# Kernel tuning notes

Measured on AMD Instinct MI355X. Metric: run time of the kernel, lower is better.

The kernel has to match this reference:

```python
import jax, jax.numpy as jnp
import numpy as np

H = 1024   # hidden_size (BERT-large)
B = 16     # bsz
L = 4      # num_label
S = 512    # seq len per (doc, option) pair
NEG = -1e30


def setup_inputs() -> dict:
    key = jax.random.key(0)
    ks = jax.random.split(key, 16)
    last_layer = jax.random.normal(ks[0], (B * L, S, H), dtype=jnp.float32)
    attention_mask = jnp.ones((B * L, S), dtype=jnp.int32)
    all_doc_final_pos = (300 + jax.random.randint(ks[1], (B * L,), 0, 150)).astype(jnp.int64)

    def w(k, shape, std=0.02):
        return jax.random.normal(k, shape, dtype=jnp.float32) * std

    return {
        "last_layer": last_layer,
        "attention_mask": attention_mask,
        "all_doc_final_pos": all_doc_final_pos,
        "num_label": L,
        "attn_w1": w(ks[2], (H,)), "attn_w2": w(ks[3], (H,)), "attn_w3": w(ks[4], (H,)),
        "opt_w1": w(ks[5], (H,)), "opt_w2": w(ks[6], (H,)), "opt_w3": w(ks[7], (H,)),
        "self_w1": w(ks[8], (H,)), "self_w2": w(ks[9], (H,)), "self_w3": w(ks[10], (H,)),
        "attn_fc_w": w(ks[11], (H, 3 * H)), "attn_fc_b": jnp.zeros((H,), jnp.float32),
        "comp_fc_w": w(ks[12], (H, 7 * H)), "comp_fc_b": jnp.zeros((H,), jnp.float32),
        "gate_fc_w": w(ks[13], (H, 2 * H)), "gate_fc_b": jnp.zeros((H,), jnp.float32),
        "self_fc_w": w(ks[14], (H, 4 * H)), "self_fc_b": jnp.zeros((H,), jnp.float32),
    }


def _trilinear(q, k, w1, w2, w3):
    # q: [b, Lq, H], k: [b, Lk, H] -> logit [b, Lq, Lk]
    q_logit = jnp.einsum('bqh,h->bq', q, w1)
    k_logit = jnp.einsum('bkh,h->bk', k, w2)
    dot = jnp.einsum('bqh,bkh->bqk', q, w3 * k)
    return q_logit[:, :, None] + k_logit[:, None, :] + dot


def _attention(q, k, v, qm, km, w1, w2, w3):
    # qm: [b, Lq] bool, km: [b, Lk] bool
    mask = qm[:, :, None] & km[:, None, :]
    logit = jnp.where(mask, _trilinear(q, k, w1, w2, w3), NEG)
    aw = jnp.where(mask, jax.nn.softmax(logit, axis=-1), 0.0)   # row softmax
    attn = jnp.matmul(aw, v)
    kq = jnp.where(mask, jax.nn.softmax(logit, axis=1), 0.0)    # column softmax
    co_w = jnp.matmul(aw, jnp.swapaxes(kq, -1, -2))             # [b, Lq, Lq]
    co_attn = jnp.matmul(co_w, q)
    return attn, co_attn


def reference(last_layer, attention_mask, all_doc_final_pos, num_label,
              attn_w1, attn_w2, attn_w3, opt_w1, opt_w2, opt_w3,
              self_w1, self_w2, self_w3,
              attn_fc_w, attn_fc_b, comp_fc_w, comp_fc_b,
              gate_fc_w, gate_fc_b, self_fc_w, self_fc_b):
    bsz = attention_mask.shape[0] // num_label
    seq = last_layer.shape[1]
    h = last_layer.shape[-1]
    ll = last_layer.reshape(bsz, num_label, seq, h)
    am = attention_mask.reshape(bsz, num_label, seq)
    fp = all_doc_final_pos.reshape(bsz, num_label)

    fp_np = np.asarray(fp)
    Ld = int(fp_np.max())          # max doc length (static)
    Lo = seq - int(fp_np.min())    # max option length (static)

    # doc: prefix [0, final_pos), zero-padded to Ld
    td = jnp.arange(Ld)
    doc_mask = (td[None, None, :] < fp[:, :, None]) & (am[:, :, :Ld] > 0)
    doc_enc = ll[:, :, :Ld, :] * doc_mask[..., None]

    # opt: suffix [final_pos, seq), zero-padded to Lo (ragged gather)
    to = jnp.arange(Lo)
    idx = fp[:, :, None] + to[None, None, :]
    valid = idx < seq
    idxc = jnp.minimum(idx, seq - 1)
    opt_enc = jnp.take_along_axis(ll, idxc[..., None], axis=2) * valid[..., None]
    opt_mask = valid & (jnp.take_along_axis(am, idxc, axis=2) > 0)

    # cross-option comparison
    corr_list = []
    for i in range(num_label):
        cur, cm = opt_enc[:, i], opt_mask[:, i]
        feats = [cur]
        for j in range(num_label):
            if j == i:
                continue
            attn, _ = _attention(cur, opt_enc[:, j], opt_enc[:, j], cm, opt_mask[:, j],
                                 opt_w1, opt_w2, opt_w3)
            feats.append(cur * attn)
            feats.append(cur - attn)
        corr_list.append(jnp.tanh(jnp.concatenate(feats, -1) @ comp_fc_w.T + comp_fc_b))
    opt_corr = jnp.stack(corr_list, axis=1).reshape(bsz * num_label, Lo, h)

    opt_mask2 = opt_mask.reshape(bsz * num_label, Lo)
    opt_enc2 = opt_enc.reshape(bsz * num_label, Lo, h)
    doc_mask2 = doc_mask.reshape(bsz * num_label, Ld)
    doc_enc2 = doc_enc.reshape(bsz * num_label, Ld, h)

    gate = jax.nn.sigmoid(jnp.concatenate([opt_enc2, opt_corr], -1) @ gate_fc_w.T + gate_fc_b)
    option = opt_enc2 * gate + opt_corr * (1.0 - gate)

    attn, coattn = _attention(option, doc_enc2, doc_enc2, opt_mask2, doc_mask2,
                              attn_w1, attn_w2, attn_w3)
    fusion = jnp.tanh(jnp.concatenate([option, attn, coattn], -1) @ attn_fc_w.T + attn_fc_b)

    attn2, _ = _attention(fusion, fusion, fusion, opt_mask2, opt_mask2,
                          self_w1, self_w2, self_w3)
    fusion = jax.nn.relu(jnp.concatenate([fusion, attn2, fusion * attn2, fusion - attn2], -1)
                         @ self_fc_w.T + self_fc_b)
    fusion = jnp.where(opt_mask2[..., None], fusion, NEG)
    return fusion.max(axis=1)
```

## Files before the change

### kernel.cpp

```cpp
#include <hip/hip_runtime.h>
#include <math.h>

#define Sv   512
#define Hv   1024
#define BSZ  16
#define NLB  4
#define NITEM 64
#define LOv  224
#define LDv  480
#define NEGV (-1e30f)
#define VTHR (-1e20f)

typedef unsigned short u16;
typedef __attribute__((ext_vector_type(8))) short short8;
using floatx4 = __attribute__((ext_vector_type(4))) float;

__device__ __forceinline__ u16 f2b(float x) {
  unsigned u = __float_as_uint(x);
  return (u16)((u + 0x7FFFu + ((u >> 16) & 1u)) >> 16);
}
__device__ __forceinline__ float b2f(u16 b) { return __uint_as_float(((unsigned)b) << 16); }

__device__ __forceinline__ float opt_view_f(const float* ll, const int* fp, int item, int t, int h) {
  int idx = fp[item] + t;
  return (idx < Sv) ? ll[((size_t)item * Sv + idx) * Hv + h] : 0.f;
}

__device__ __forceinline__ void gll16(const u16* g, u16* l) {
  __builtin_amdgcn_global_load_lds(
      (const __attribute__((address_space(1))) unsigned int*)(const void*)g,
      (__attribute__((address_space(3))) unsigned int*)(void*)l, 16, 0, 0);
}

__device__ __forceinline__ int swz(int r) { return (r >> 1) & 3; }

enum { EP_BF16 = 0, EP_LOGIT = 1, EP_AS = 2 };
enum { IX_INST = 0, IX_ITQ = 1, IX_ITK = 2 };

struct MG {
  const u16* A; long long sA; int lda; int aidx;
  const u16* B; long long sB; int ldb; int bidx;
  float* C; long long sC; int ldc; int cidx;
  u16* Cb;
  const unsigned char* qmask; int ldqm;
  const unsigned char* kmask; int ldkm;
  const float* qlogv; int ldql;
  const float* klogv; int ldkl;
  int M, N, K, qi, kj, epi, pm;
};

__global__ __launch_bounds__(256) void mgemm(MG p) {
  __shared__ u16 As[128][32];
  __shared__ u16 Bs[128][32];
  int inst = blockIdx.z;
  int itq, itk;
  if (p.pm) {
    int b = inst % BSZ, pair = inst / BSZ;
    int i = pair / 3, jj = pair % 3;
    int j = jj + (jj >= i ? 1 : 0);
    itq = b * NLB + i; itk = b * NLB + j;
  } else {
    itq = (p.qi >= 0) ? inst * NLB + p.qi : inst;
    itk = (p.kj >= 0) ? inst * NLB + p.kj : inst;
  }
  int ai = (p.aidx == IX_ITQ) ? itq : (p.aidx == IX_ITK ? itk : inst);
  int bi = (p.bidx == IX_ITQ) ? itq : (p.bidx == IX_ITK ? itk : inst);
  int ci = (p.cidx == IX_ITQ) ? itq : (p.cidx == IX_ITK ? itk : inst);
  const u16* Ab = p.A + (size_t)ai * p.sA;
  const u16* Bb = p.B + (size_t)bi * p.sB;
  int tid = threadIdx.x;
  int m0 = blockIdx.y * 128, n0 = blockIdx.x * 128;
  int wave = tid >> 6, lane = tid & 63;
  int wm = (wave >> 1) * 64, wn = (wave & 1) * 64;
  int col = lane & 15, quad = lane >> 4;
  int rl = lane >> 2, cslot = lane & 3;
  floatx4 acc[4][4] = {};

  {
    uint4 z4 = {0, 0, 0, 0};
    uint4* a4 = (uint4*)&As[0][0];
    uint4* b4 = (uint4*)&Bs[0][0];
    for (int z = tid; z < 512; z += 256) { a4[z] = z4; b4[z] = z4; }
  }
  __syncthreads();

  for (int k0 = 0; k0 < p.K; k0 += 32) {
    int rb = wave * 32;
    #pragma unroll
    for (int c = 0; c < 2; c++) {
      int r = rb + c * 16 + rl;
      int gk = k0 + ((cslot ^ swz(r)) * 8);
      if (m0 + r < p.M) gll16(Ab + (size_t)(m0 + r) * p.lda + gk, &As[rb + c * 16][0]);
      if (n0 + r < p.N) gll16(Bb + (size_t)(n0 + r) * p.ldb + gk, &Bs[rb + c * 16][0]);
    }
    __syncthreads();
    short8 a[4], b[4];
    #pragma unroll
    for (int mi = 0; mi < 4; mi++) {
      int r = wm + mi * 16 + col;
      a[mi] = *(const short8*)&As[r][(quad ^ swz(r)) * 8];
    }
    #pragma unroll
    for (int ni = 0; ni < 4; ni++) {
      int r = wn + ni * 16 + col;
      b[ni] = *(const short8*)&Bs[r][(quad ^ swz(r)) * 8];
    }
    #pragma unroll
    for (int mi = 0; mi < 4; mi++)
      #pragma unroll
      for (int ni = 0; ni < 4; ni++)
        acc[mi][ni] = __builtin_amdgcn_mfma_f32_16x16x32_bf16(a[mi], b[ni], acc[mi][ni], 0, 0, 0);
    __syncthreads();
  }

  int sblk = (inst / BSZ) % 3;
  #pragma unroll
  for (int mi = 0; mi < 4; mi++) {
    #pragma unroll
    for (int ni = 0; ni < 4; ni++) {
      int n = n0 + wn + ni * 16 + col;
      if (n >= p.N) continue;
      #pragma unroll
      for (int r = 0; r < 4; r++) {
        int m = m0 + wm + mi * 16 + quad * 4 + r;
        if (m >= p.M) continue;
        float v = acc[mi][ni][r];
        if (p.epi == EP_BF16) {
          p.Cb[(size_t)ci * p.sC + (size_t)m * p.ldc + n] = f2b(v);
        } else if (p.epi == EP_AS) {
          u16* base = p.Cb + (size_t)itq * p.sC + (size_t)m * p.ldc;
          float cur = b2f(base[n]);
          base[(size_t)(1 + 2 * sblk) * Hv + n] = f2b(cur * v);
          base[(size_t)(2 + 2 * sblk) * Hv + n] = f2b(cur - v);
        } else {
          bool qm = p.qmask[itq * p.ldqm + m] != 0;
          bool km = p.kmask[itk * p.ldkm + n] != 0;
          p.C[(size_t)ci * p.sC + (size_t)m * p.ldc + n] =
            (qm && km) ? (v + p.qlogv[(size_t)itq * p.ldql + m] + p.klogv[(size_t)itk * p.ldkl + n]) : NEGV;
        }
      }
    }
  }
}

enum { FCE_TANH = 0, FCE_GATE = 1, FCE_SELFMAX = 2 };

struct MF {
  const u16* A; long long sA;
  const u16* B;
  float* C; long long sC;
  const float* bias;
  const float* ll; const int* fp; const float* Yv;
  const unsigned char* optm; float* outmax;
  int M, K, epi;
};

__global__ __launch_bounds__(256) void mgemm_fc(MF p) {
  __shared__ u16 As[128][32];
  __shared__ u16 Bs[128][32];
  int id = blockIdx.x;
  int low = id & 7, nt = (id >> 3) & 7, hi = id >> 6;
  int g = (hi << 3) | low;
  int inst = g >> 1, mt = g & 1;
  const u16* Ab = p.A + (size_t)inst * p.sA;
  int tid = threadIdx.x;
  int m0 = mt * 128, n0 = nt * 128;
  int wave = tid >> 6, lane = tid & 63;
  int wm = (wave >> 1) * 64, wn = (wave & 1) * 64;
  int col = lane & 15, quad = lane >> 4;
  int rl = lane >> 2, cslot = lane & 3;
  floatx4 acc[4][4] = {};

  {
    uint4 z4 = {0, 0, 0, 0};
    uint4* a4 = (uint4*)&As[0][0];
    uint4* b4 = (uint4*)&Bs[0][0];
    for (int z = tid; z < 512; z += 256) { a4[z] = z4; b4[z] = z4; }
  }
  __syncthreads();

  for (int k0 = 0; k0 < p.K; k0 += 32) {
    int rb = wave * 32;
    #pragma unroll
    for (int c = 0; c < 2; c++) {
      int r = rb + c * 16 + rl;
      int gk = k0 + ((cslot ^ swz(r)) * 8);
      if (m0 + r < p.M) gll16(Ab + (size_t)(m0 + r) * p.K + gk, &As[rb + c * 16][0]);
      gll16(p.B + (size_t)(n0 + r) * p.K + gk, &Bs[rb + c * 16][0]);
    }
    __syncthreads();
    short8 a[4], b[4];
    #pragma unroll
    for (int mi = 0; mi < 4; mi++) {
      int r = wm + mi * 16 + col;
      a[mi] = *(const short8*)&As[r][(quad ^ swz(r)) * 8];
    }
    #pragma unroll
    for (int ni = 0; ni < 4; ni++) {
      int r = wn + ni * 16 + col;
      b[ni] = *(const short8*)&Bs[r][(quad ^ swz(r)) * 8];
    }
    #pragma unroll
    for (int mi = 0; mi < 4; mi++)
      #pragma unroll
      for (int ni = 0; ni < 4; ni++)
        acc[mi][ni] = __builtin_amdgcn_mfma_f32_16x16x32_bf16(a[mi], b[ni], acc[mi][ni], 0, 0, 0);
    __syncthreads();
  }

  if (p.epi == FCE_SELFMAX) {
    #pragma unroll
    for (int ni = 0; ni < 4; ni++) {
      int n = n0 + wn + ni * 16 + col;
      float bn = p.bias[n];
      float mloc = 0.f;
      #pragma unroll
      for (int mi = 0; mi < 4; mi++)
        #pragma unroll
        for (int r = 0; r < 4; r++) {
          int m = m0 + wm + mi * 16 + quad * 4 + r;
          float vv = fmaxf(acc[mi][ni][r] + bn, 0.f);
          if (m < p.M && p.optm[inst * LOv + m]) mloc = fmaxf(mloc, vv);
        }
      mloc = fmaxf(mloc, __shfl_xor(mloc, 16, 64));
      mloc = fmaxf(mloc, __shfl_xor(mloc, 32, 64));
      if (quad == 0)
        atomicMax((unsigned int*)(p.outmax + (size_t)inst * Hv + n), __float_as_uint(mloc));
    }
    return;
  }
  #pragma unroll
  for (int mi = 0; mi < 4; mi++) {
    #pragma unroll
    for (int ni = 0; ni < 4; ni++) {
      int n = n0 + wn + ni * 16 + col;
      #pragma unroll
      for (int r = 0; r < 4; r++) {
        int m = m0 + wm + mi * 16 + quad * 4 + r;
        if (m >= p.M) continue;
        float v = acc[mi][ni][r] + p.bias[n];
        float* cp = p.C + (size_t)inst * p.sC + (size_t)m * Hv + n;
        if (p.epi == FCE_TANH) {
          *cp = tanhf(v);
        } else {
          float gg = 1.f / (1.f + __expf(-v));
          float xv = opt_view_f(p.ll, p.fp, inst, m, n);
          float yv = p.Yv[(size_t)inst * p.sC + (size_t)m * Hv + n];
          *cp = xv * gg + yv * (1.f - gg);
        }
      }
    }
  }
}

__global__ __launch_bounds__(256) void init_masks(const int* fp_in, const int* am, int* fp,
                                                  unsigned char* optm, unsigned char* docm) {
  int item = blockIdx.x;
  int f = fp_in[item];
  if (threadIdx.x == 0) fp[item] = f;
  for (int t = threadIdx.x; t < LDv; t += blockDim.x) {
    docm[item * LDv + t] = (t < f && t < Sv && am[item * Sv + t] > 0) ? 1 : 0;
    if (t < LOv) {
      int idx = f + t;
      optm[item * LOv + t] = (idx < Sv && am[item * Sv + idx] > 0) ? 1 : 0;
    }
  }
}

__global__ __launch_bounds__(256) void convf2b(const float* src, u16* dst, int n) {
  int i = blockIdx.x * 256 + threadIdx.x;
  int stride = gridDim.x * 256;
  for (; i < n; i += stride) dst[i] = f2b(src[i]);
}

__global__ __launch_bounds__(256) void build_opt(const float* ll, const int* fp, const float* w3,
                                                 u16* compA0, u16* optw3B) {
  int t = blockIdx.x, item = blockIdx.y;
  int idx = fp[item] + t;
  bool v = idx < Sv;
  const float* src = ll + ((size_t)item * Sv + (v ? idx : 0)) * Hv;
  u16* d0 = compA0 + ((size_t)item * LOv + t) * (7 * Hv);
  u16* d1 = optw3B + ((size_t)item * LOv + t) * Hv;
  for (int h = threadIdx.x; h < Hv; h += 256) {
    float x = v ? src[h] : 0.f;
    d0[h] = f2b(x);
    d1[h] = f2b(x * w3[h]);
  }
}

__global__ __launch_bounds__(256) void build_doc(const float* ll, const unsigned char* docm, u16* docB) {
  int t = blockIdx.x, item = blockIdx.y;
  bool v = docm[item * LDv + t] != 0;
  const float* src = ll + ((size_t)item * Sv + (t < Sv ? t : 0)) * Hv;
  size_t o = ((size_t)item * LDv + t) * Hv;
  for (int h = threadIdx.x; h < Hv; h += 256) docB[o + h] = v ? f2b(src[h]) : (u16)0;
}

__global__ __launch_bounds__(256) void transpose_b(const float* src, long long sS,
                                                   const float* ll, const int* fp, const unsigned char* docm,
                                                   int mode, int Lt, u16* out) {
  __shared__ float tile[32][33];
  int t0 = blockIdx.x * 32, h0 = blockIdx.y * 32, item = blockIdx.z;
  int tx = threadIdx.x & 31, ty0 = threadIdx.x >> 5;
  for (int yy = ty0; yy < 32; yy += 8) {
    int t = t0 + yy, h = h0 + tx;
    float v = 0.f;
    if (t < Lt) {
      if (mode == 0)      v = src[(size_t)item * sS + (size_t)t * Hv + h];
      else if (mode == 1) { int idx = fp[item] + t; if (idx < Sv) v = ll[((size_t)item * Sv + idx) * Hv + h]; }
      else                { if (docm[item * LDv + t]) v = ll[((size_t)item * Sv + t) * Hv + h]; }
    }
    tile[yy][tx] = v;
  }
  __syncthreads();
  for (int yy = ty0; yy < 32; yy += 8) {
    int h = h0 + yy, t = t0 + tx;
    if (t < Lt) out[((size_t)item * Hv + h) * (size_t)Lt + t] = f2b(tile[tx][yy]);
  }
}

__global__ __launch_bounds__(256) void build_gateA(const float* ll, const int* fp, const float* corr, u16* gateA) {
  int t = blockIdx.x, item = blockIdx.y;
  int idx = fp[item] + t;
  bool v = idx < Sv;
  const float* src = ll + ((size_t)item * Sv + (v ? idx : 0)) * Hv;
  u16* dst = gateA + ((size_t)item * LOv + t) * (2 * Hv);
  const float* cr = corr + ((size_t)item * LOv + t) * Hv;
  for (int h = threadIdx.x; h < Hv; h += 256) {
    dst[h] = f2b(v ? src[h] : 0.f);
    dst[Hv + h] = f2b(cr[h]);
  }
}

__global__ __launch_bounds__(256) void conv_act(const float* src, const float* w3,
                                                u16* dst1, int ld1, u16* dstw3) {
  int t = blockIdx.x, item = blockIdx.y;
  const float* s = src + ((size_t)item * LOv + t) * Hv;
  u16* d1 = dst1 + ((size_t)item * LOv + t) * ld1;
  u16* d2 = dstw3 + ((size_t)item * LOv + t) * Hv;
  for (int h = threadIdx.x; h < Hv; h += 256) {
    float x = s[h];
    d1[h] = f2b(x);
    d2[h] = f2b(x * w3[h]);
  }
}

__global__ __launch_bounds__(256) void build_selfA23(u16* selfA) {
  int t = blockIdx.x, item = blockIdx.y;
  u16* row = selfA + ((size_t)item * LOv + t) * (4 * Hv);
  for (int h = threadIdx.x; h < Hv; h += 256) {
    float f = b2f(row[h]), a = b2f(row[Hv + h]);
    row[2 * Hv + h] = f2b(f * a);
    row[3 * Hv + h] = f2b(f - a);
  }
}

__global__ __launch_bounds__(256) void dot_rows(const float* src, long long sS,
                                                const float* ll, const int* fp, const unsigned char* docm,
                                                const float* w, float* outv, int ldo, int mode) {
  int t = blockIdx.x, item = blockIdx.y;
  int tid = threadIdx.x;
  float s = 0.f;
  for (int h = tid; h < Hv; h += 256) {
    float v;
    if (mode == 0)      v = src[(size_t)item * sS + (size_t)t * Hv + h];
    else if (mode == 1) v = opt_view_f(ll, fp, item, t, h);
    else                v = docm[item * LDv + t] ? ll[((size_t)item * Sv + t) * Hv + h] : 0.f;
    s += v * w[h];
  }
  __shared__ float red[4];
  for (int o = 32; o > 0; o >>= 1) s += __shfl_down(s, o, 64);
  int lane = tid & 63, wv = tid >> 6;
  if (lane == 0) red[wv] = s;
  __syncthreads();
  if (tid == 0) outv[(size_t)item * ldo + t] = red[0] + red[1] + red[2] + red[3];
}

__global__ __launch_bounds__(256) void row_softmax(const float* src, u16* dst, int Lk, int ldl, long long sL) {
  int m = blockIdx.x, inst = blockIdx.y;
  const float* row = src + (size_t)inst * sL + (size_t)m * ldl;
  u16* orow = dst + (size_t)inst * sL + (size_t)m * ldl;
  int tid = threadIdx.x;
  float mx = -INFINITY;
  for (int t = tid; t < Lk; t += 256) mx = fmaxf(mx, row[t]);
  __shared__ float sm[4]; __shared__ float ss[4];
  for (int o = 32; o > 0; o >>= 1) mx = fmaxf(mx, __shfl_down(mx, o, 64));
  int lane = tid & 63, wv = tid >> 6;
  if (lane == 0) sm[wv] = mx;
  __syncthreads();
  mx = fmaxf(fmaxf(sm[0], sm[1]), fmaxf(sm[2], sm[3]));
  float sum = 0.f;
  for (int t = tid; t < Lk; t += 256) sum += __expf(row[t] - mx);
  for (int o = 32; o > 0; o >>= 1) sum += __shfl_down(sum, o, 64);
  if (lane == 0) ss[wv] = sum;
  __syncthreads();
  sum = ss[0] + ss[1] + ss[2] + ss[3];
  float inv = 1.f / sum;
  for (int t = tid; t < Lk; t += 256) {
    float x = row[t];
    orow[t] = (x < VTHR) ? (u16)0 : f2b(__expf(x - mx) * inv);
  }
}

__global__ __launch_bounds__(256) void col_softmax(const float* src, u16* dst, int Mr, int ldl, long long sL) {
  int c = blockIdx.x, inst = blockIdx.y;
  const float* base = src + (size_t)inst * sL + c;
  u16* ob = dst + (size_t)inst * sL + c;
  int tid = threadIdx.x;
  float mx = -INFINITY;
  for (int t = tid; t < Mr; t += 256) mx = fmaxf(mx, base[(size_t)t * ldl]);
  __shared__ float sm[4]; __shared__ float ss[4];
  for (int o = 32; o > 0; o >>= 1) mx = fmaxf(mx, __shfl_down(mx, o, 64));
  int lane = tid & 63, wv = tid >> 6;
  if (lane == 0) sm[wv] = mx;
  __syncthreads();
  mx = fmaxf(fmaxf(sm[0], sm[1]), fmaxf(sm[2], sm[3]));
  float sum = 0.f;
  for (int t = tid; t < Mr; t += 256) sum += __expf(base[(size_t)t * ldl] - mx);
  for (int o = 32; o > 0; o >>= 1) sum += __shfl_down(sum, o, 64);
  if (lane == 0) ss[wv] = sum;
  __syncthreads();
  sum = ss[0] + ss[1] + ss[2] + ss[3];
  float inv = 1.f / sum;
  for (int t = tid; t < Mr; t += 256) {
    float x = base[(size_t)t * ldl];
    ob[(size_t)t * ldl] = (x < VTHR) ? (u16)0 : f2b(__expf(x - mx) * inv);
  }
}

extern "C" void kernel_launch(void* const* d_in, const int* in_sizes, int n_in,
                              void* d_out, int out_size, void* d_ws, size_t ws_size,
                              hipStream_t stream) {
  const float* ll        = (const float*)d_in[0];
  const int* am          = (const int*)d_in[1];
  const int* fp_in       = (const int*)d_in[2];
  const float* attn_w1   = (const float*)d_in[4];
  const float* attn_w2   = (const float*)d_in[5];
  const float* attn_w3   = (const float*)d_in[6];
  const float* opt_w1    = (const float*)d_in[7];
  const float* opt_w2    = (const float*)d_in[8];
  const float* opt_w3    = (const float*)d_in[9];
  const float* self_w1   = (const float*)d_in[10];
  const float* self_w2   = (const float*)d_in[11];
  const float* self_w3   = (const float*)d_in[12];
  const float* attn_fc_w = (const float*)d_in[13];
  const float* attn_fc_b = (const float*)d_in[14];
  const float* comp_fc_w = (const float*)d_in[15];
  const float* comp_fc_b = (const float*)d_in[16];
  const float* gate_fc_w = (const float*)d_in[17];
  const float* gate_fc_b = (const float*)d_in[18];
  const float* self_fc_w = (const float*)d_in[19];
  const float* self_fc_b = (const float*)d_in[20];
  float* out = (float*)d_out;

  const size_t BIGF = (size_t)NITEM * LOv * Hv;
  float* optcorrF = (float*)d_ws;
  float* optionF  = optcorrF + BIGF;
  float* logitF   = optionF + BIGF;
  float* qlog     = logitF + BIGF;
  float* klog     = qlog + (size_t)NITEM * LOv;
  float* optq     = klog + (size_t)NITEM * LDv;
  float* optk     = optq + (size_t)NITEM * LOv;
  u16* wcomp = (u16*)(optk + (size_t)NITEM * LOv);
  u16* wgate = wcomp + (size_t)Hv * 7 * Hv;
  u16* wattn = wgate + (size_t)Hv * 2 * Hv;
  u16* wself = wattn + (size_t)Hv * 3 * Hv;
  u16* kqB   = wself + (size_t)Hv * 4 * Hv;
  u16* awbB  = kqB + (size_t)NITEM * LOv * LDv;
  u16* cowB  = awbB + (size_t)NITEM * LOv * LDv;
  unsigned char* optm = (unsigned char*)(cowB + (size_t)NITEM * LOv * LOv);
  unsigned char* docm = optm + (size_t)NITEM * LOv;
  int* fp = (int*)(docm + (size_t)NITEM * LDv);
  u16* U = (u16*)(fp + NITEM + 32);
  const size_t E_OPT = (size_t)NITEM * LOv * Hv;
  const size_t E_DOC = (size_t)NITEM * LDv * Hv;
  u16* optw3B = U;
  u16* optTB  = U + E_OPT;
  u16* aw1B   = U + 2 * E_OPT;
  u16* compA  = aw1B + (size_t)12 * BSZ * LOv * LOv;
  u16* gateA  = U;
  u16* docB   = U;
  u16* docTB  = U + E_DOC;
  u16* optw3C = U + 2 * E_DOC;
  u16* optTC  = optw3C + E_OPT;
  u16* attnA  = optTC + E_OPT;
  u16* selfA  = U;
  u16* fusw3  = U + (size_t)NITEM * LOv * 4 * Hv;
  u16* fusTB  = fusw3 + E_OPT;
  float* fusionF = optcorrF;

  const long long sOH = (long long)LOv * Hv;
  const long long sLL = (long long)LOv * LOv;
  const long long sLD = (long long)LOv * LDv;
  const long long sC7 = (long long)LOv * 7 * Hv;

  (void)hipMemsetAsync(d_out, 0, (size_t)NITEM * Hv * sizeof(float), stream);
  init_masks<<<NITEM, 256, 0, stream>>>(fp_in, am, fp, optm, docm);
  convf2b<<<1024, 256, 0, stream>>>(comp_fc_w, wcomp, Hv * 7 * Hv);
  convf2b<<<1024, 256, 0, stream>>>(gate_fc_w, wgate, Hv * 2 * Hv);
  convf2b<<<1024, 256, 0, stream>>>(attn_fc_w, wattn, Hv * 3 * Hv);
  convf2b<<<1024, 256, 0, stream>>>(self_fc_w, wself, Hv * 4 * Hv);
  build_opt<<<dim3(LOv, NITEM), 256, 0, stream>>>(ll, fp, opt_w3, compA, optw3B);
  transpose_b<<<dim3(LOv / 32, Hv / 32, NITEM), 256, 0, stream>>>(nullptr, 0, ll, fp, docm, 1, LOv, optTB);
  dot_rows<<<dim3(LOv, NITEM), 256, 0, stream>>>(nullptr, 0, ll, fp, docm, opt_w1, optq, LOv, 1);
  dot_rows<<<dim3(LOv, NITEM), 256, 0, stream>>>(nullptr, 0, ll, fp, docm, opt_w2, optk, LOv, 1);

  {
    MG p = {};
    p.A = optw3B; p.sA = sOH; p.lda = Hv; p.aidx = IX_ITQ;
    p.B = compA;  p.sB = sC7; p.ldb = 7 * Hv; p.bidx = IX_ITK;
    p.C = logitF; p.sC = sLL; p.ldc = LOv; p.cidx = IX_INST;
    p.qmask = optm; p.ldqm = LOv; p.kmask = optm; p.ldkm = LOv;
    p.qlogv = optq; p.ldql = LOv; p.klogv = optk; p.ldkl = LOv;
    p.M = LOv; p.N = LOv; p.K = Hv; p.epi = EP_LOGIT; p.pm = 1;
    mgemm<<<dim3(2, 2, 12 * BSZ), 256, 0, stream>>>(p);
  }
  row_softmax<<<dim3(LOv, 12 * BSZ), 256, 0, stream>>>(logitF, aw1B, LOv, LOv, sLL);
  {
    MG p = {};
    p.A = aw1B; p.sA = sLL; p.lda = LOv; p.aidx = IX_INST;
    p.B = optTB; p.sB = (long long)Hv * LOv; p.ldb = LOv; p.bidx = IX_ITK;
    p.Cb = compA; p.sC = sC7; p.ldc = 7 * Hv; p.cidx = IX_ITQ;
    p.M = LOv; p.N = Hv; p.K = LOv; p.epi = EP_AS; p.pm = 1;
    mgemm<<<dim3(8, 2, 12 * BSZ), 256, 0, stream>>>(p);
  }
  {
    MF p = {};
    p.A = compA; p.sA = sC7; p.B = wcomp;
    p.C = optcorrF; p.sC = sOH; p.bias = comp_fc_b;
    p.M = LOv; p.K = 7 * Hv; p.epi = FCE_TANH;
    mgemm_fc<<<1024, 256, 0, stream>>>(p);
  }

  build_gateA<<<dim3(LOv, NITEM), 256, 0, stream>>>(ll, fp, optcorrF, gateA);
  {
    MF p = {};
    p.A = gateA; p.sA = (long long)LOv * 2 * Hv; p.B = wgate;
    p.C = optionF; p.sC = sOH; p.bias = gate_fc_b;
    p.ll = ll; p.fp = fp; p.Yv = optcorrF;
    p.M = LOv; p.K = 2 * Hv; p.epi = FCE_GATE;
    mgemm_fc<<<1024, 256, 0, stream>>>(p);
  }

  build_doc<<<dim3(LDv, NITEM), 256, 0, stream>>>(ll, docm, docB);
  transpose_b<<<dim3(LDv / 32, Hv / 32, NITEM), 256, 0, stream>>>(nullptr, 0, ll, fp, docm, 2, LDv, docTB);
  conv_act<<<dim3(LOv, NITEM), 256, 0, stream>>>(optionF, attn_w3, attnA, 3 * Hv, optw3C);
  transpose_b<<<dim3(LOv / 32, Hv / 32, NITEM), 256, 0, stream>>>(optionF, sOH, ll, fp, docm, 0, LOv, optTC);
  dot_rows<<<dim3(LOv, NITEM), 256, 0, stream>>>(optionF, sOH, ll, fp, docm, attn_w1, qlog, LOv, 0);
  dot_rows<<<dim3(LDv, NITEM), 256, 0, stream>>>(nullptr, 0, ll, fp, docm, attn_w2, klog, LDv, 2);
  {
    MG p = {};
    p.A = optw3C; p.sA = sOH; p.lda = Hv; p.aidx = IX_INST;
    p.B = docB; p.sB = (long long)LDv * Hv; p.ldb = Hv; p.bidx = IX_INST;
    p.C = logitF; p.sC = sLD; p.ldc = LDv; p.cidx = IX_INST;
    p.qmask = optm; p.ldqm = LOv; p.kmask = docm; p.ldkm = LDv;
    p.qlogv = qlog; p.ldql = LOv; p.klogv = klog; p.ldkl = LDv;
    p.M = LOv; p.N = LDv; p.K = Hv; p.qi = -1; p.kj = -1; p.epi = EP_LOGIT;
    mgemm<<<dim3(4, 2, NITEM), 256, 0, stream>>>(p);
  }
  row_softmax<<<dim3(LOv, NITEM), 256, 0, stream>>>(logitF, awbB, LDv, LDv, sLD);
  col_softmax<<<dim3(LDv, NITEM), 256, 0, stream>>>(logitF, kqB, LOv, LDv, sLD);
  {
    MG p = {};
    p.A = awbB; p.sA = sLD; p.lda = LDv; p.aidx = IX_INST;
    p.B = docTB; p.sB = (long long)Hv * LDv; p.ldb = LDv; p.bidx = IX_INST;
    p.Cb = attnA + Hv; p.sC = (long long)LOv * 3 * Hv; p.ldc = 3 * Hv; p.cidx = IX_INST;
    p.M = LOv; p.N = Hv; p.K = LDv; p.qi = -1; p.kj = -1; p.epi = EP_BF16;
    mgemm<<<dim3(8, 2, NITEM), 256, 0, stream>>>(p);
  }
  {
    MG p = {};
    p.A = awbB; p.sA = sLD; p.lda = LDv; p.aidx = IX_INST;
    p.B = kqB; p.sB = sLD; p.ldb = LDv; p.bidx = IX_INST;
    p.Cb = cowB; p.sC = sLL; p.ldc = LOv; p.cidx = IX_INST;
    p.M = LOv; p.N = LOv; p.K = LDv; p.qi = -1; p.kj = -1; p.epi = EP_BF16;
    mgemm<<<dim3(2, 2, NITEM), 256, 0, stream>>>(p);
  }
  {
    MG p = {};
    p.A = cowB; p.sA = sLL; p.lda = LOv; p.aidx = IX_INST;
    p.B = optTC; p.sB = (long long)Hv * LOv; p.ldb = LOv; p.bidx = IX_INST;
    p.Cb = attnA + 2 * Hv; p.sC = (long long)LOv * 3 * Hv; p.ldc = 3 * Hv; p.cidx = IX_INST;
    p.M = LOv; p.N = Hv; p.K = LOv; p.qi = -1; p.kj = -1; p.epi = EP_BF16;
    mgemm<<<dim3(8, 2, NITEM), 256, 0, stream>>>(p);
  }
  {
    MF p = {};
    p.A = attnA; p.sA = (long long)LOv * 3 * Hv; p.B = wattn;
    p.C = fusionF; p.sC = sOH; p.bias = attn_fc_b;
    p.M = LOv; p.K = 3 * Hv; p.epi = FCE_TANH;
    mgemm_fc<<<1024, 256, 0, stream>>>(p);
  }

  conv_act<<<dim3(LOv, NITEM), 256, 0, stream>>>(fusionF, self_w3, selfA, 4 * Hv, fusw3);
  transpose_b<<<dim3(LOv / 32, Hv / 32, NITEM), 256, 0, stream>>>(fusionF, sOH, ll, fp, docm, 0, LOv, fusTB);
  dot_rows<<<dim3(LOv, NITEM), 256, 0, stream>>>(fusionF, sOH, ll, fp, docm, self_w1, qlog, LOv, 0);
  dot_rows<<<dim3(LOv, NITEM), 256, 0, stream>>>(fusionF, sOH, ll, fp, docm, self_w2, klog, LOv, 0);
  {
    MG p = {};
    p.A = fusw3; p.sA = sOH; p.lda = Hv; p.aidx = IX_INST;
    p.B = selfA; p.sB = (long long)LOv * 4 * Hv; p.ldb = 4 * Hv; p.bidx = IX_INST;
    p.C = logitF; p.sC = sLL; p.ldc = LOv; p.cidx = IX_INST;
    p.qmask = optm; p.ldqm = LOv; p.kmask = optm; p.ldkm = LOv;
    p.qlogv = qlog; p.ldql = LOv; p.klogv = klog; p.ldkl = LOv;
    p.M = LOv; p.N = LOv; p.K = Hv; p.qi = -1; p.kj = -1; p.epi = EP_LOGIT;
    mgemm<<<dim3(2, 2, NITEM), 256, 0, stream>>>(p);
  }
  row_softmax<<<dim3(LOv, NITEM), 256, 0, stream>>>(logitF, awbB, LOv, LOv, sLL);
  {
    MG p = {};
    p.A = awbB; p.sA = sLL; p.lda = LOv; p.aidx = IX_INST;
    p.B = fusTB; p.sB = (long long)Hv * LOv; p.ldb = LOv; p.bidx = IX_INST;
    p.Cb = selfA + Hv; p.sC = (long long)LOv * 4 * Hv; p.ldc = 4 * Hv; p.cidx = IX_INST;
    p.M = LOv; p.N = Hv; p.K = LOv; p.qi = -1; p.kj = -1; p.epi = EP_BF16;
    mgemm<<<dim3(8, 2, NITEM), 256, 0, stream>>>(p);
  }
  build_selfA23<<<dim3(LOv, NITEM), 256, 0, stream>>>(selfA);
  {
    MF p = {};
    p.A = selfA; p.sA = (long long)LOv * 4 * Hv; p.B = wself;
    p.bias = self_fc_b; p.optm = optm; p.outmax = out;
    p.M = LOv; p.K = 4 * Hv; p.epi = FCE_SELFMAX;
    mgemm_fc<<<1024, 256, 0, stream>>>(p);
  }
}
```

Baseline: 2.298 ms.

## Double-buffer LDS tiles in GEMM kernels to overlap loads with MFMA

Both GEMM kernels now use two LDS buffers for the A and B tiles. The next k-slice is prefetched into the alternate buffer while MFMAs run on the current one, and one barrier per iteration is dropped. This aims to hide global-to-LDS load latency behind the matrix math. It doubles the LDS use per block, which may reduce occupancy, and the overlap depends on how the compiler places its waits for the asynchronous loads.

```diff
diff --git a/kernel.cpp b/kernel.cpp
--- a/kernel.cpp
+++ b/kernel.cpp
@@ -50,8 +50,8 @@
 };
 
 __global__ __launch_bounds__(256) void mgemm(MG p) {
-  __shared__ u16 As[128][32];
-  __shared__ u16 Bs[128][32];
+  __shared__ u16 As[2][128][32];
+  __shared__ u16 Bs[2][128][32];
   int inst = blockIdx.z;
   int itq, itk;
   if (p.pm) {
@@ -78,39 +78,51 @@
 
   {
     uint4 z4 = {0, 0, 0, 0};
-    uint4* a4 = (uint4*)&As[0][0];
-    uint4* b4 = (uint4*)&Bs[0][0];
-    for (int z = tid; z < 512; z += 256) { a4[z] = z4; b4[z] = z4; }
-  }
-  __syncthreads();
-
-  for (int k0 = 0; k0 < p.K; k0 += 32) {
-    int rb = wave * 32;
-    #pragma unroll
-    for (int c = 0; c < 2; c++) {
-      int r = rb + c * 16 + rl;
-      int gk = k0 + ((cslot ^ swz(r)) * 8);
-      if (m0 + r < p.M) gll16(Ab + (size_t)(m0 + r) * p.lda + gk, &As[rb + c * 16][0]);
-      if (n0 + r < p.N) gll16(Bb + (size_t)(n0 + r) * p.ldb + gk, &Bs[rb + c * 16][0]);
-    }
+    uint4* a4 = (uint4*)&As[0][0][0];
+    uint4* b4 = (uint4*)&Bs[0][0][0];
+    for (int z = tid; z < 1024; z += 256) { a4[z] = z4; b4[z] = z4; }
+  }
+  __syncthreads();
+
+  int rb = wave * 32;
+  int nk = p.K >> 5;
+  #pragma unroll
+  for (int c = 0; c < 2; c++) {
+    int r = rb + c * 16 + rl;
+    int gk = (cslot ^ swz(r)) * 8;
+    if (m0 + r < p.M) gll16(Ab + (size_t)(m0 + r) * p.lda + gk, &As[0][rb + c * 16][0]);
+    if (n0 + r < p.N) gll16(Bb + (size_t)(n0 + r) * p.ldb + gk, &Bs[0][rb + c * 16][0]);
+  }
+  int cur = 0;
+  for (int ks = 0; ks < nk; ks++) {
     __syncthreads();
+    if (ks + 1 < nk) {
+      int k0 = (ks + 1) << 5;
+      #pragma unroll
+      for (int c = 0; c < 2; c++) {
+        int r = rb + c * 16 + rl;
+        int gk = k0 + ((cslot ^ swz(r)) * 8);
+        if (m0 + r < p.M) gll16(Ab + (size_t)(m0 + r) * p.lda + gk, &As[cur ^ 1][rb + c * 16][0]);
+        if (n0 + r < p.N) gll16(Bb + (size_t)(n0 + r) * p.ldb + gk, &Bs[cur ^ 1][rb + c * 16][0]);
+      }
+    }
     short8 a[4], b[4];
     #pragma unroll
     for (int mi = 0; mi < 4; mi++) {
       int r = wm + mi * 16 + col;
-      a[mi] = *(const short8*)&As[r][(quad ^ swz(r)) * 8];
+      a[mi] = *(const short8*)&As[cur][r][(quad ^ swz(r)) * 8];
     }
     #pragma unroll
     for (int ni = 0; ni < 4; ni++) {
       int r = wn + ni * 16 + col;
-      b[ni] = *(const short8*)&Bs[r][(quad ^ swz(r)) * 8];
+      b[ni] = *(const short8*)&Bs[cur][r][(quad ^ swz(r)) * 8];
     }
     #pragma unroll
     for (int mi = 0; mi < 4; mi++)
       #pragma unroll
       for (int ni = 0; ni < 4; ni++)
         acc[mi][ni] = __builtin_amdgcn_mfma_f32_16x16x32_bf16(a[mi], b[ni], acc[mi][ni], 0, 0, 0);
-    __syncthreads();
+    cur ^= 1;
   }
 
   int sblk = (inst / BSZ) % 3;
@@ -129,9 +141,9 @@
           p.Cb[(size_t)ci * p.sC + (size_t)m * p.ldc + n] = f2b(v);
         } else if (p.epi == EP_AS) {
           u16* base = p.Cb + (size_t)itq * p.sC + (size_t)m * p.ldc;
-          float cur = b2f(base[n]);
-          base[(size_t)(1 + 2 * sblk) * Hv + n] = f2b(cur * v);
-          base[(size_t)(2 + 2 * sblk) * Hv + n] = f2b(cur - v);
+          float cur2 = b2f(base[n]);
+          base[(size_t)(1 + 2 * sblk) * Hv + n] = f2b(cur2 * v);
+          base[(size_t)(2 + 2 * sblk) * Hv + n] = f2b(cur2 - v);
         } else {
           bool qm = p.qmask[itq * p.ldqm + m] != 0;
           bool km = p.kmask[itk * p.ldkm + n] != 0;
@@ -156,8 +168,8 @@
 };
 
 __global__ __launch_bounds__(256) void mgemm_fc(MF p) {
-  __shared__ u16 As[128][32];
-  __shared__ u16 Bs[128][32];
+  __shared__ u16 As[2][128][32];
+  __shared__ u16 Bs[2][128][32];
   int id = blockIdx.x;
   int low = id & 7, nt = (id >> 3) & 7, hi = id >> 6;
   int g = (hi << 3) | low;
@@ -173,39 +185,51 @@
 
   {
     uint4 z4 = {0, 0, 0, 0};
-    uint4* a4 = (uint4*)&As[0][0];
-    uint4* b4 = (uint4*)&Bs[0][0];
-    for (int z = tid; z < 512; z += 256) { a4[z] = z4; b4[z] = z4; }
-  }
-  __syncthreads();
-
-  for (int k0 = 0; k0 < p.K; k0 += 32) {
-    int rb = wave * 32;
-    #pragma unroll
-    for (int c = 0; c < 2; c++) {
-      int r = rb + c * 16 + rl;
-      int gk = k0 + ((cslot ^ swz(r)) * 8);
-      if (m0 + r < p.M) gll16(Ab + (size_t)(m0 + r) * p.K + gk, &As[rb + c * 16][0]);
-      gll16(p.B + (size_t)(n0 + r) * p.K + gk, &Bs[rb + c * 16][0]);
-    }
+    uint4* a4 = (uint4*)&As[0][0][0];
+    uint4* b4 = (uint4*)&Bs[0][0][0];
+    for (int z = tid; z < 1024; z += 256) { a4[z] = z4; b4[z] = z4; }
+  }
+  __syncthreads();
+
+  int rb = wave * 32;
+  int nk = p.K >> 5;
+  #pragma unroll
+  for (int c = 0; c < 2; c++) {
+    int r = rb + c * 16 + rl;
+    int gk = (cslot ^ swz(r)) * 8;
+    if (m0 + r < p.M) gll16(Ab + (size_t)(m0 + r) * p.K + gk, &As[0][rb + c * 16][0]);
+    gll16(p.B + (size_t)(n0 + r) * p.K + gk, &Bs[0][rb + c * 16][0]);
+  }
+  int cur = 0;
+  for (int ks = 0; ks < nk; ks++) {
     __syncthreads();
+    if (ks + 1 < nk) {
+      int k0 = (ks + 1) << 5;
+      #pragma unroll
+      for (int c = 0; c < 2; c++) {
+        int r = rb + c * 16 + rl;
+        int gk = k0 + ((cslot ^ swz(r)) * 8);
+        if (m0 + r < p.M) gll16(Ab + (size_t)(m0 + r) * p.K + gk, &As[cur ^ 1][rb + c * 16][0]);
+        gll16(p.B + (size_t)(n0 + r) * p.K + gk, &Bs[cur ^ 1][rb + c * 16][0]);
+      }
+    }
     short8 a[4], b[4];
     #pragma unroll
     for (int mi = 0; mi < 4; mi++) {
       int r = wm + mi * 16 + col;
-      a[mi] = *(const short8*)&As[r][(quad ^ swz(r)) * 8];
+      a[mi] = *(const short8*)&As[cur][r][(quad ^ swz(r)) * 8];
     }
     #pragma unroll
     for (int ni = 0; ni < 4; ni++) {
       int r = wn + ni * 16 + col;
-      b[ni] = *(const short8*)&Bs[r][(quad ^ swz(r)) * 8];
+      b[ni] = *(const short8*)&Bs[cur][r][(quad ^ swz(r)) * 8];
     }
     #pragma unroll
     for (int mi = 0; mi < 4; mi++)
       #pragma unroll
       for (int ni = 0; ni < 4; ni++)
         acc[mi][ni] = __builtin_amdgcn_mfma_f32_16x16x32_bf16(a[mi], b[ni], acc[mi][ni], 0, 0, 0);
-    __syncthreads();
+    cur ^= 1;
   }
 
   if (p.epi == FCE_SELFMAX) {
```

After: 2.323 ms. No clear change (+1.1%).
